# Performance work log

Hardware: AMD Instinct MI355X
Metric: run time of the kernel (lower is better)

Reference implementation:

```python
import jax, jax.numpy as jnp
import numpy as np

B, C = 65536, 1000
EPS = float(np.finfo(np.float32).eps)

def setup_inputs() -> dict:
    key = jax.random.key(0)
    k1, k2, k3 = jax.random.split(key, 3)
    return {
        "Simple_vector": jax.random.normal(k1, (B, C), dtype=jnp.float32),
        "label_list": jax.random.randint(k2, (B,), 0, C),
        "w_L": jax.random.normal(k3, (C,), dtype=jnp.float32),
        "w_H": jnp.ones((1,), dtype=jnp.float32),
        "b": jnp.ones((1,), dtype=jnp.float32),
    }

def reference(Simple_vector, label_list, w_L, w_H, b):
    C_ = Simple_vector.shape[1]
    # LTS: per-row dot with class-weight vector
    LTS = Simple_vector @ w_L  # (B,)
    # H_hat = sum_i p_i * log p_i  (negative entropy), single stable pass
    logp = jax.nn.log_softmax(Simple_vector, axis=1)
    H_hat = jnp.sum(jnp.exp(logp) * logp, axis=1)  # (B,)
    HTS = w_H[0] * (H_hat / jnp.log(jnp.float32(C_))) + b[0]
    a = LTS + HTS
    T = jnp.clip(jax.nn.softplus(a), EPS, None)  # (B,)
    scaled = Simple_vector / T[:, None]
    # mean cross-entropy
    ls = jax.nn.log_softmax(scaled, axis=1)
    nll = -jnp.take_along_axis(ls, label_list[:, None], axis=1)[:, 0]
    return jnp.mean(nll)
```

## Files before the change

kernel.cpp:

```cpp
#include <hip/hip_runtime.h>
#include <float.h>
#include <math.h>


static constexpr int   kC4    = 250;
static constexpr int   kBlock = 256;
static constexpr int   kGrid  = 1280;
static constexpr int   kWavesTotal = kGrid * (kBlock / 64);
static constexpr float kEps   = 1.1920928955078125e-07f;
static constexpr float kLogC  = 6.907755279f;

__device__ __forceinline__ float wred_max(float v) {
#pragma unroll
  for (int off = 32; off > 0; off >>= 1) v = fmaxf(v, __shfl_xor(v, off, 64));
  return v;
}
__device__ __forceinline__ float wred_sum(float v) {
#pragma unroll
  for (int off = 32; off > 0; off >>= 1) v += __shfl_xor(v, off, 64);
  return v;
}
__device__ __forceinline__ void wred_sum3(float& a, float& b, float& c) {
#pragma unroll
  for (int off = 32; off > 0; off >>= 1) {
    float ta = __shfl_xor(a, off, 64);
    float tb = __shfl_xor(b, off, 64);
    float tc = __shfl_xor(c, off, 64);
    a += ta; b += tb; c += tc;
  }
}

__device__ __forceinline__ void p1_dot_max(const float4 c, const float4 w,
                                           float& L, float& m) {
  L = fmaf(c.x, w.x, L); L = fmaf(c.y, w.y, L);
  L = fmaf(c.z, w.z, L); L = fmaf(c.w, w.w, L);
  m = fmaxf(m, fmaxf(fmaxf(c.x, c.y), fmaxf(c.z, c.w)));
}
__device__ __forceinline__ void p2_sumexp(const float4 c, const float m,
                                          float& S, float& W) {
  float e;
  e = __expf(c.x - m); S += e; W = fmaf(e, c.x, W);
  e = __expf(c.y - m); S += e; W = fmaf(e, c.y, W);
  e = __expf(c.z - m); S += e; W = fmaf(e, c.z, W);
  e = __expf(c.w - m); S += e; W = fmaf(e, c.w, W);
}
__device__ __forceinline__ void p3_sumexp2(const float4 c, const float rT,
                                           const float nmrT, float& S2) {
  S2 += __expf(fmaf(c.x, rT, nmrT)); S2 += __expf(fmaf(c.y, rT, nmrT));
  S2 += __expf(fmaf(c.z, rT, nmrT)); S2 += __expf(fmaf(c.w, rT, nmrT));
}

#define SENT4 make_float4(-FLT_MAX, -FLT_MAX, -FLT_MAX, -FLT_MAX)

__global__ __launch_bounds__(kBlock, 5) void ats_row_kernel(
    const float* __restrict__ X, const int* __restrict__ labels,
    const float* __restrict__ wL, const float* __restrict__ wH,
    const float* __restrict__ bb, double* __restrict__ partial, int B) {
  const int lane   = threadIdx.x & 63;
  const int wib    = threadIdx.x >> 6;
  const int wid    = blockIdx.x * (kBlock / 64) + wib;
  const bool tailok = lane < (kC4 - 192);

  const float4* WLr = reinterpret_cast<const float4*>(wL);
  const float wH0 = wH[0];
  const float b0  = bb[0];

  double acc = 0.0;

  int row = wid;
  float4 c0, c1, c2, c3;
  int labc = 0;
  if (row < B) {
    const float4* Xr = reinterpret_cast<const float4*>(X) + (size_t)row * kC4;
    c0 = Xr[lane]; c1 = Xr[64 + lane]; c2 = Xr[128 + lane];
    c3 = tailok ? Xr[192 + lane] : SENT4;
    labc = labels[row];
  }

  for (; row < B; row += kWavesTotal) {
    const int nrow = row + kWavesTotal;
    float4 n0 = SENT4, n1 = SENT4, n2 = SENT4, n3 = SENT4;
    int labn = 0;
    if (nrow < B) {
      const float4* Xn = reinterpret_cast<const float4*>(X) + (size_t)nrow * kC4;
      n0 = Xn[lane]; n1 = Xn[64 + lane]; n2 = Xn[128 + lane];
      n3 = tailok ? Xn[192 + lane] : SENT4;
      labn = labels[nrow];
    }
    const float4 w0 = WLr[lane];
    const float4 w1 = WLr[64 + lane];
    const float4 w2 = WLr[128 + lane];
    const float4 w3 = tailok ? WLr[192 + lane] : make_float4(0.f, 0.f, 0.f, 0.f);

    float L = 0.f, m = -FLT_MAX;
    p1_dot_max(c0, w0, L, m); p1_dot_max(c1, w1, L, m);
    p1_dot_max(c2, w2, L, m); p1_dot_max(c3, w3, L, m);
    m = wred_max(m);

    float S = 0.f, W = 0.f;
    p2_sumexp(c0, m, S, W); p2_sumexp(c1, m, S, W);
    p2_sumexp(c2, m, S, W); p2_sumexp(c3, m, S, W);
    wred_sum3(S, W, L);

    const int c4l = labc >> 2;
    const int sl  = c4l >> 6, ln = c4l & 63, el = labc & 3;
    float4 v = (sl == 0) ? c0 : (sl == 1) ? c1 : (sl == 2) ? c2 : c3;
    float cand = (el == 0) ? v.x : (el == 1) ? v.y : (el == 2) ? v.z : v.w;
    const float xl = __shfl(cand, ln, 64);

    const float Hhat = W / S - m - __logf(S);
    const float a    = L + wH0 * (Hhat / kLogC) + b0;
    const float sp   = (a > 0.f) ? (a + log1pf(__expf(-a))) : log1pf(__expf(a));
    const float T    = fmaxf(sp, kEps);
    const float rT   = 1.0f / T;
    const float nmrT = -m * rT;

    float S2 = 0.f;
    p3_sumexp2(c0, rT, nmrT, S2); p3_sumexp2(c1, rT, nmrT, S2);
    p3_sumexp2(c2, rT, nmrT, S2); p3_sumexp2(c3, rT, nmrT, S2);
    S2 = wred_sum(S2);

    const float nll = __logf(S2) - fmaf(xl, rT, nmrT);
    acc += (double)nll;

    c0 = n0; c1 = n1; c2 = n2; c3 = n3; labc = labn;
  }

  __shared__ double sacc[kBlock / 64];
  if (lane == 0) sacc[wib] = acc;
  __syncthreads();
  if (threadIdx.x == 0)
    partial[blockIdx.x] = (sacc[0] + sacc[1]) + (sacc[2] + sacc[3]);
}

__global__ __launch_bounds__(256) void ats_final_kernel(
    const double* __restrict__ partial, float* __restrict__ out, int n, int B) {
  __shared__ double sdata[256];
  double a = 0.0;
  for (int i = threadIdx.x; i < n; i += 256) a += partial[i];
  sdata[threadIdx.x] = a;
  __syncthreads();
#pragma unroll
  for (int s = 128; s > 0; s >>= 1) {
    if ((int)threadIdx.x < s) sdata[threadIdx.x] += sdata[threadIdx.x + s];
    __syncthreads();
  }
  if (threadIdx.x == 0) out[0] = (float)(sdata[0] / (double)B);
}

extern "C" void kernel_launch(void* const* d_in, const int* in_sizes, int n_in,
                              void* d_out, int out_size, void* d_ws, size_t ws_size,
                              hipStream_t stream) {
  (void)n_in; (void)out_size; (void)ws_size;
  const float* X   = (const float*)d_in[0];
  const int*   lab = (const int*)d_in[1];
  const float* wL  = (const float*)d_in[2];
  const float* wH  = (const float*)d_in[3];
  const float* bb  = (const float*)d_in[4];
  const int B = in_sizes[1];
  double* partial = (double*)d_ws;
  float* out = (float*)d_out;

  ats_row_kernel<<<kGrid, kBlock, 0, stream>>>(X, lab, wL, wH, bb, partial, B);
  ats_final_kernel<<<1, 256, 0, stream>>>(partial, out, kGrid, B);
}
```

Measured before the change: 66.14 us.

## Use packed float2 math, hoist weight loads, enlarge grid, relax launch bounds

Result: no change. 65.32 us (-1.2%).

```diff
diff --git a/kernel.cpp b/kernel.cpp
--- a/kernel.cpp
+++ b/kernel.cpp
@@ -5,10 +5,12 @@
 
 static constexpr int   kC4    = 250;
 static constexpr int   kBlock = 256;
-static constexpr int   kGrid  = 1280;
+static constexpr int   kGrid  = 2048;
 static constexpr int   kWavesTotal = kGrid * (kBlock / 64);
 static constexpr float kEps   = 1.1920928955078125e-07f;
 static constexpr float kLogC  = 6.907755279f;
+
+typedef float v2f __attribute__((ext_vector_type(2)));
 
 __device__ __forceinline__ float wred_max(float v) {
 #pragma unroll
@@ -23,36 +25,47 @@
 __device__ __forceinline__ void wred_sum3(float& a, float& b, float& c) {
 #pragma unroll
   for (int off = 32; off > 0; off >>= 1) {
-    float ta = __shfl_xor(a, off, 64);
-    float tb = __shfl_xor(b, off, 64);
-    float tc = __shfl_xor(c, off, 64);
+    const float ta = __shfl_xor(a, off, 64);
+    const float tb = __shfl_xor(b, off, 64);
+    const float tc = __shfl_xor(c, off, 64);
     a += ta; b += tb; c += tc;
   }
 }
 
 __device__ __forceinline__ void p1_dot_max(const float4 c, const float4 w,
-                                           float& L, float& m) {
-  L = fmaf(c.x, w.x, L); L = fmaf(c.y, w.y, L);
-  L = fmaf(c.z, w.z, L); L = fmaf(c.w, w.w, L);
-  m = fmaxf(m, fmaxf(fmaxf(c.x, c.y), fmaxf(c.z, c.w)));
+                                           v2f& Lp, v2f& mp) {
+  const v2f clo = {c.x, c.y}, chi = {c.z, c.w};
+  const v2f wlo = {w.x, w.y}, whi = {w.z, w.w};
+  Lp = __builtin_elementwise_fma(clo, wlo, Lp);
+  Lp = __builtin_elementwise_fma(chi, whi, Lp);
+  mp = __builtin_elementwise_max(mp, __builtin_elementwise_max(clo, chi));
 }
 __device__ __forceinline__ void p2_sumexp(const float4 c, const float m,
-                                          float& S, float& W) {
-  float e;
-  e = __expf(c.x - m); S += e; W = fmaf(e, c.x, W);
-  e = __expf(c.y - m); S += e; W = fmaf(e, c.y, W);
-  e = __expf(c.z - m); S += e; W = fmaf(e, c.z, W);
-  e = __expf(c.w - m); S += e; W = fmaf(e, c.w, W);
+                                          v2f& Sp, v2f& Wp) {
+  v2f e, x;
+  x.x = c.x; x.y = c.y;
+  e.x = __expf(c.x - m); e.y = __expf(c.y - m);
+  Sp += e;  Wp = __builtin_elementwise_fma(e, x, Wp);
+  x.x = c.z; x.y = c.w;
+  e.x = __expf(c.z - m); e.y = __expf(c.w - m);
+  Sp += e;  Wp = __builtin_elementwise_fma(e, x, Wp);
 }
-__device__ __forceinline__ void p3_sumexp2(const float4 c, const float rT,
-                                           const float nmrT, float& S2) {
-  S2 += __expf(fmaf(c.x, rT, nmrT)); S2 += __expf(fmaf(c.y, rT, nmrT));
-  S2 += __expf(fmaf(c.z, rT, nmrT)); S2 += __expf(fmaf(c.w, rT, nmrT));
+__device__ __forceinline__ void p3_sumexp2(const float4 c, const v2f rT2,
+                                           const v2f nmrT2, v2f& S2p) {
+  v2f x, a, e;
+  x.x = c.x; x.y = c.y;
+  a = __builtin_elementwise_fma(x, rT2, nmrT2);
+  e.x = __expf(a.x); e.y = __expf(a.y);
+  S2p += e;
+  x.x = c.z; x.y = c.w;
+  a = __builtin_elementwise_fma(x, rT2, nmrT2);
+  e.x = __expf(a.x); e.y = __expf(a.y);
+  S2p += e;
 }
 
 #define SENT4 make_float4(-FLT_MAX, -FLT_MAX, -FLT_MAX, -FLT_MAX)
 
-__global__ __launch_bounds__(kBlock, 5) void ats_row_kernel(
+__global__ __launch_bounds__(kBlock) void ats_row_kernel(
     const float* __restrict__ X, const int* __restrict__ labels,
     const float* __restrict__ wL, const float* __restrict__ wH,
     const float* __restrict__ bb, double* __restrict__ partial, int B) {
@@ -62,6 +75,10 @@
   const bool tailok = lane < (kC4 - 192);
 
   const float4* WLr = reinterpret_cast<const float4*>(wL);
+  const float4 w0 = WLr[lane];
+  const float4 w1 = WLr[64 + lane];
+  const float4 w2 = WLr[128 + lane];
+  const float4 w3 = tailok ? WLr[192 + lane] : make_float4(0.f, 0.f, 0.f, 0.f);
   const float wH0 = wH[0];
   const float b0  = bb[0];
 
@@ -69,8 +86,8 @@
 
   int row = wid;
   float4 c0, c1, c2, c3;
-  int labc = 0;
-  if (row < B) {
+  int labc;
+  {
     const float4* Xr = reinterpret_cast<const float4*>(X) + (size_t)row * kC4;
     c0 = Xr[lane]; c1 = Xr[64 + lane]; c2 = Xr[128 + lane];
     c3 = tailok ? Xr[192 + lane] : SENT4;
@@ -87,19 +104,17 @@
       n3 = tailok ? Xn[192 + lane] : SENT4;
       labn = labels[nrow];
     }
-    const float4 w0 = WLr[lane];
-    const float4 w1 = WLr[64 + lane];
-    const float4 w2 = WLr[128 + lane];
-    const float4 w3 = tailok ? WLr[192 + lane] : make_float4(0.f, 0.f, 0.f, 0.f);
 
-    float L = 0.f, m = -FLT_MAX;
-    p1_dot_max(c0, w0, L, m); p1_dot_max(c1, w1, L, m);
-    p1_dot_max(c2, w2, L, m); p1_dot_max(c3, w3, L, m);
-    m = wred_max(m);
+    v2f Lp = {0.f, 0.f}, mp = {-FLT_MAX, -FLT_MAX};
+    p1_dot_max(c0, w0, Lp, mp); p1_dot_max(c1, w1, Lp, mp);
+    p1_dot_max(c2, w2, Lp, mp); p1_dot_max(c3, w3, Lp, mp);
+    float L = Lp.x + Lp.y;
+    float m = wred_max(fmaxf(mp.x, mp.y));
 
-    float S = 0.f, W = 0.f;
-    p2_sumexp(c0, m, S, W); p2_sumexp(c1, m, S, W);
-    p2_sumexp(c2, m, S, W); p2_sumexp(c3, m, S, W);
+    v2f Sp = {0.f, 0.f}, Wp = {0.f, 0.f};
+    p2_sumexp(c0, m, Sp, Wp); p2_sumexp(c1, m, Sp, Wp);
+    p2_sumexp(c2, m, Sp, Wp); p2_sumexp(c3, m, Sp, Wp);
+    float S = Sp.x + Sp.y, W = Wp.x + Wp.y;
     wred_sum3(S, W, L);
 
     const int c4l = labc >> 2;
@@ -114,11 +129,13 @@
     const float T    = fmaxf(sp, kEps);
     const float rT   = 1.0f / T;
     const float nmrT = -m * rT;
+    const v2f rT2   = {rT, rT};
+    const v2f nmrT2 = {nmrT, nmrT};
 
-    float S2 = 0.f;
-    p3_sumexp2(c0, rT, nmrT, S2); p3_sumexp2(c1, rT, nmrT, S2);
-    p3_sumexp2(c2, rT, nmrT, S2); p3_sumexp2(c3, rT, nmrT, S2);
-    S2 = wred_sum(S2);
+    v2f S2p = {0.f, 0.f};
+    p3_sumexp2(c0, rT2, nmrT2, S2p); p3_sumexp2(c1, rT2, nmrT2, S2p);
+    p3_sumexp2(c2, rT2, nmrT2, S2p); p3_sumexp2(c3, rT2, nmrT2, S2p);
+    float S2 = wred_sum(S2p.x + S2p.y);
 
     const float nll = __logf(S2) - fmaf(xl, rT, nmrT);
     acc += (double)nll;
```
